# Performance work log

Hardware: AMD Instinct MI355X
Metric: run time of the kernel (lower is better)

## Reference

```python
import jax, jax.numpy as jnp
import numpy as np

N, IN, H, C, E = 20000, 256, 256, 16, 640000

def sage_conv(x, edge_index, W_l, b_l, W_r):
    # PyG SAGEConv (aggr='mean', root_weight=True):
    # out = lin_l(mean_{j in N(i)} x_j) + lin_r(x_i)
    src, dst = edge_index[0], edge_index[1]
    n = x.shape[0]
    msgs = x[src]                                            # [E, d] irregular gather
    agg = jax.ops.segment_sum(msgs, dst, num_segments=n)     # [N, d]
    deg = jax.ops.segment_sum(jnp.ones((msgs.shape[0],), x.dtype), dst, num_segments=n)
    agg = agg / jnp.maximum(deg, 1.0)[:, None]               # mean aggregation
    return agg @ W_l + b_l + x @ W_r


def setup_inputs() -> dict:
    key = jax.random.key(0)
    ks = jax.random.split(key, 10)
    s = lambda k, fi, fo: jax.random.normal(k, (fi, fo), jnp.float32) / np.sqrt(fi)
    return {
        "x": jax.random.normal(ks[0], (N, IN), jnp.float32),
        "edge_index": jax.random.randint(ks[1], (2, E), 0, N, jnp.int64),
        "W1l": s(ks[2], IN, H), "b1": jnp.zeros((H,), jnp.float32), "W1r": s(ks[3], IN, H),
        "W2l": s(ks[4], H, H),  "b2": jnp.zeros((H,), jnp.float32), "W2r": s(ks[5], H, H),
        "Wc": s(ks[6], H, C),   "bc": jnp.zeros((C,), jnp.float32),
    }


def reference(x, edge_index, W1l, b1, W1r, W2l, b2, W2r, Wc, bc):
    h = sage_conv(x, edge_index, W1l, b1, W1r)
    h = jax.nn.relu(h)                    # dropout is identity in eval mode
    z = sage_conv(h, edge_index, W2l, b2, W2r)
    return z @ Wc + bc                    # classifier logits [N, C]
```

## Files before the change

### kernel.cpp

```cpp
#include <hip/hip_runtime.h>
#include <hip/hip_bf16.h>


#define FEAT 256
#define NCLS 16
#define ZPAD 264
#define NSH  8
#define SCAP 64
#define SLOTS (NSH * SCAP)
#define CAPTOT 128

typedef __bf16 bf16x8 __attribute__((ext_vector_type(8)));
typedef __bf16 bf16x4 __attribute__((ext_vector_type(4)));
typedef float  f32x4  __attribute__((ext_vector_type(4)));
typedef float  f32x2  __attribute__((ext_vector_type(2)));
typedef unsigned int uint4v __attribute__((ext_vector_type(4)));

#define ACC8(S, U) do {                                                   \
    _Pragma("unroll")                                                     \
    for (int w_ = 0; w_ < 4; ++w_) {                                      \
        f32x2 lo_ = __builtin_amdgcn_cvt_pk_f32_fp8(U[w_], false);        \
        f32x2 hi_ = __builtin_amdgcn_cvt_pk_f32_fp8(U[w_], true);         \
        S[w_][0] += lo_[0]; S[w_][1] += lo_[1];                           \
        S[w_][2] += hi_[0]; S[w_][3] += hi_[1];                           \
    } } while (0)

__device__ __forceinline__ void load_entries(
    const int* __restrict__ cnt, const unsigned short* __restrict__ bucket,
    int node, int lane, int& e0, int& e1, int& deg, float& inv)
{
    int4 ca = *(const int4*)(cnt + node * NSH);
    int4 cb = *(const int4*)(cnt + node * NSH + 4);
    int cs[NSH] = {ca.x, ca.y, ca.z, ca.w, cb.x, cb.y, cb.z, cb.w};
    int ctrue = 0, d = 0;
    #pragma unroll
    for (int s = 0; s < NSH; ++s) {
        ctrue += cs[s];
        cs[s] = cs[s] < SCAP ? cs[s] : SCAP;
        d += cs[s];
    }
    deg = d < CAPTOT ? d : CAPTOT;
    inv = ctrue > 0 ? 1.0f / (float)ctrue : 0.0f;
    const unsigned short* lst = bucket + (size_t)node * SLOTS;

    auto get = [&](int i) -> int {
        int s = 0, loc = i;
        #pragma unroll
        for (int t = 0; t < NSH - 1; ++t) {
            if (s == t && loc >= cs[t]) { loc -= cs[t]; s = t + 1; }
        }
        return lst[s * SCAP + loc];
    };
    e0 = (lane < deg)      ? get(lane)      : 0;
    e1 = (lane + 64 < deg) ? get(lane + 64) : 0;
}


__global__ void combo_kernel(const float* __restrict__ x,
                             const float* __restrict__ W1l, const float* __restrict__ W1r,
                             const float* __restrict__ W2l, const float* __restrict__ W2r,
                             const float* __restrict__ Wc, const float* __restrict__ b2,
                             const float* __restrict__ bc,
                             const int* __restrict__ src, const int* __restrict__ dst,
                             __bf16* __restrict__ xb, unsigned char* __restrict__ x8,
                             __bf16* __restrict__ W1lT, __bf16* __restrict__ W1rT,
                             __bf16* __restrict__ WaT, __bf16* __restrict__ WbT,
                             float* __restrict__ bc2,
                             int* __restrict__ cnt, unsigned short* __restrict__ bucket,
                             int n4, int E, int nb_cvt) {
    int t = threadIdx.x;
    int bx = blockIdx.x;
    if (bx < nb_cvt) {
        int i = bx * 256 + t;
        if (i < n4) {
            f32x4 v = ((const f32x4*)x)[i];
            bf16x4 o;
            #pragma unroll
            for (int j = 0; j < 4; ++j) o[j] = (__bf16)v[j];
            ((bf16x4*)xb)[i] = o;
            int pk = 0;
            pk = __builtin_amdgcn_cvt_pk_fp8_f32(v[0], v[1], pk, false);
            pk = __builtin_amdgcn_cvt_pk_fp8_f32(v[2], v[3], pk, true);
            ((int*)x8)[i] = pk;
        }
    } else if (bx < nb_cvt + 512) {
        int b = bx - nb_cvt;
        int w = b >> 8, nn = b & 255;
        const float* W = w ? W1r : W1l;
        __bf16* WT = w ? W1rT : W1lT;
        WT[nn * FEAT + t] = (__bf16)W[t * FEAT + nn];
    } else if (bx < nb_cvt + 512 + 32) {
        int b = bx - nb_cvt - 512;
        int c = b & 15;
        const float* W = (b < 16) ? W2l : W2r;
        __bf16* WT = (b < 16) ? WaT : WbT;
        float s = 0.f;
        #pragma unroll 4
        for (int m = 0; m < FEAT; ++m)
            s += W[t * FEAT + m] * Wc[m * NCLS + c];
        WT[c * FEAT + t] = (__bf16)s;
    } else if (bx == nb_cvt + 512 + 32) {
        if (t < NCLS) {
            float s = 0.f;
            for (int k = 0; k < FEAT; ++k) s += b2[k] * Wc[k * NCLS + t];
            bc2[t] = s + bc[t];
        }
    } else {
        int sh = bx & (NSH - 1);
        int idx = (bx - nb_cvt - 512 - 33) * 256 + t;
        int e2 = idx * 2;
        if (e2 < E) {
            int2 sv = *(const int2*)(src + e2);
            int2 dv = *(const int2*)(dst + e2);
            int p0 = atomicAdd(&cnt[dv.x * NSH + sh], 1);
            if (p0 < SCAP) bucket[(size_t)dv.x * SLOTS + sh * SCAP + p0] = (unsigned short)sv.x;
            if (e2 + 1 < E) {
                int p1 = atomicAdd(&cnt[dv.y * NSH + sh], 1);
                if (p1 < SCAP) bucket[(size_t)dv.y * SLOTS + sh * SCAP + p1] = (unsigned short)sv.y;
            }
        }
    }
}


__global__ __launch_bounds__(256) void agg_fp8_kernel(
    const unsigned char* __restrict__ t8, const int* __restrict__ cnt,
    const unsigned short* __restrict__ bucket, __bf16* __restrict__ out, int n)
{
    int wave = threadIdx.x >> 6;
    int node = blockIdx.x * 4 + wave;
    if (node >= n) return;
    int lane = threadIdx.x & 63;
    int quad = lane >> 4, l16 = lane & 15;

    int e0, e1, deg; float inv;
    load_entries(cnt, bucket, node, lane, e0, e1, deg, inv);

    f32x4 s0[4], s1[4];
    #pragma unroll
    for (int w = 0; w < 4; ++w) { s0[w] = (f32x4){0.f,0.f,0.f,0.f}; s1[w] = (f32x4){0.f,0.f,0.f,0.f}; }

    int nfull = deg >> 2;
    int rem   = deg & 3;
    const unsigned char* base = t8 + l16 * 16;

    int tt = 0;
    for (; tt + 3 < nfull; tt += 4) {
        int i0 = (tt + 0) * 4 + quad, i1 = (tt + 1) * 4 + quad;
        int i2 = (tt + 2) * 4 + quad, i3 = (tt + 3) * 4 + quad;
        int j0 = (i0 < 64) ? __shfl(e0, i0) : __shfl(e1, i0 - 64);
        int j1 = (i1 < 64) ? __shfl(e0, i1) : __shfl(e1, i1 - 64);
        int j2 = (i2 < 64) ? __shfl(e0, i2) : __shfl(e1, i2 - 64);
        int j3 = (i3 < 64) ? __shfl(e0, i3) : __shfl(e1, i3 - 64);
        uint4v u0 = *(const uint4v*)(base + (size_t)j0 * FEAT);
        uint4v u1 = *(const uint4v*)(base + (size_t)j1 * FEAT);
        uint4v u2 = *(const uint4v*)(base + (size_t)j2 * FEAT);
        uint4v u3 = *(const uint4v*)(base + (size_t)j3 * FEAT);
        ACC8(s0, u0); ACC8(s1, u1); ACC8(s0, u2); ACC8(s1, u3);
    }
    for (; tt < nfull; ++tt) {
        int i = tt * 4 + quad;
        int j = (i < 64) ? __shfl(e0, i) : __shfl(e1, i - 64);
        uint4v u = *(const uint4v*)(base + (size_t)j * FEAT);
        ACC8(s0, u);
    }
    if (rem) {
        int i = nfull * 4 + quad;
        int j = (i < 64) ? __shfl(e0, i) : __shfl(e1, i - 64);
        if (quad < rem) {
            uint4v u = *(const uint4v*)(base + (size_t)j * FEAT);
            ACC8(s1, u);
        }
    }

    #pragma unroll
    for (int w = 0; w < 4; ++w)
        #pragma unroll
        for (int j = 0; j < 4; ++j) {
            float v = s0[w][j] + s1[w][j];
            v += __shfl_xor(v, 16, 64);
            v += __shfl_xor(v, 32, 64);
            s0[w][j] = v;
        }

    bf16x4 o;
    #pragma unroll
    for (int j = 0; j < 4; ++j) o[j] = (__bf16)(s0[quad][j] * inv);
    *(bf16x4*)(out + (size_t)node * FEAT + l16 * 16 + quad * 4) = o;
}


__global__ __launch_bounds__(256) void gemm1_kernel(
    const __bf16* __restrict__ A1, const __bf16* __restrict__ A2,
    const __bf16* __restrict__ B1T, const __bf16* __restrict__ B2T,
    const float* __restrict__ bias,
    const __bf16* __restrict__ WaT, const __bf16* __restrict__ WbT,
    const float* __restrict__ bc2,
    __bf16* __restrict__ pb, float* __restrict__ q, int M)
{
    __shared__ __align__(16) __bf16 tile[32][ZPAD];

    int m0   = blockIdx.x * 32;
    int lane = threadIdx.x & 63;
    int wave = threadIdx.x >> 6;
    int l16  = lane & 15, quad = lane >> 4;

    f32x4 acc[2][4];
    #pragma unroll
    for (int a = 0; a < 2; ++a)
        #pragma unroll
        for (int b = 0; b < 4; ++b) acc[a][b] = (f32x4){0.f, 0.f, 0.f, 0.f};

    int arow[2];
    #pragma unroll
    for (int mt = 0; mt < 2; ++mt) {
        int r = m0 + mt * 16 + l16;
        arow[mt] = (r < M) ? r : (M - 1);
    }
    int nbase = wave * 64;

    for (int pass = 0; pass < 2; ++pass) {
        const __bf16* A  = pass ? A2 : A1;
        const __bf16* BT = pass ? B2T : B1T;
        #pragma unroll 2
        for (int kk = 0; kk < 8; ++kk) {
            int k0 = kk * 32 + quad * 8;
            bf16x8 af[2], bfm[4];
            #pragma unroll
            for (int mt = 0; mt < 2; ++mt)
                af[mt] = *(const bf16x8*)(A + (size_t)arow[mt] * FEAT + k0);
            #pragma unroll
            for (int nt = 0; nt < 4; ++nt)
                bfm[nt] = *(const bf16x8*)(BT + (size_t)(nbase + nt * 16 + l16) * FEAT + k0);
            #pragma unroll
            for (int mt = 0; mt < 2; ++mt)
                #pragma unroll
                for (int nt = 0; nt < 4; ++nt)
                    acc[mt][nt] = __builtin_amdgcn_mfma_f32_16x16x32_bf16(
                        af[mt], bfm[nt], acc[mt][nt], 0, 0, 0);
        }
    }

    #pragma unroll
    for (int nt = 0; nt < 4; ++nt) {
        int col = nbase + nt * 16 + l16;
        float bv = bias[col];
        #pragma unroll
        for (int mt = 0; mt < 2; ++mt) {
            int lr = mt * 16 + quad * 4;
            #pragma unroll
            for (int r = 0; r < 4; ++r) {
                float v = acc[mt][nt][r] + bv;
                tile[lr + r][col] = (__bf16)(v > 0.f ? v : 0.f);
            }
        }
    }
    __syncthreads();

    {
        int half = wave >> 1;
        int lr = half * 16 + l16;
        const __bf16* WT = (wave & 1) ? WbT : WaT;
        f32x4 a = {0.f, 0.f, 0.f, 0.f};
        #pragma unroll
        for (int kk = 0; kk < 8; ++kk) {
            int k0 = kk * 32 + quad * 8;
            bf16x8 av = *(const bf16x8*)(&tile[lr][k0]);
            bf16x8 bv = *(const bf16x8*)(WT + (size_t)l16 * FEAT + k0);
            a = __builtin_amdgcn_mfma_f32_16x16x32_bf16(av, bv, a, 0, 0, 0);
        }
        if (wave & 1) {
            float qv = bc2[l16];
            #pragma unroll
            for (int r = 0; r < 4; ++r) {
                int row = m0 + half * 16 + quad * 4 + r;
                if (row < M) q[(size_t)row * NCLS + l16] = a[r] + qv;
            }
        } else {
            #pragma unroll
            for (int r = 0; r < 4; ++r) {
                int row = m0 + half * 16 + quad * 4 + r;
                if (row < M) pb[(size_t)row * NCLS + l16] = (__bf16)a[r];
            }
        }
    }
}


__global__ __launch_bounds__(256) void agg_out_kernel(
    const __bf16* __restrict__ pb, const float* __restrict__ q,
    const int* __restrict__ cnt, const unsigned short* __restrict__ bucket,
    float* __restrict__ out, int n)
{
    int wave = threadIdx.x >> 6;
    int node = blockIdx.x * 4 + wave;
    if (node >= n) return;
    int lane = threadIdx.x & 63;
    int quad = lane >> 4, l16 = lane & 15;

    int e0, e1, deg; float inv;
    load_entries(cnt, bucket, node, lane, e0, e1, deg, inv);

    float s0 = 0.f, s1 = 0.f;
    int nfull = deg >> 2;
    int rem   = deg & 3;

    int tt = 0;
    for (; tt + 3 < nfull; tt += 4) {
        int i0 = (tt + 0) * 4 + quad, i1 = (tt + 1) * 4 + quad;
        int i2 = (tt + 2) * 4 + quad, i3 = (tt + 3) * 4 + quad;
        int j0 = (i0 < 64) ? __shfl(e0, i0) : __shfl(e1, i0 - 64);
        int j1 = (i1 < 64) ? __shfl(e0, i1) : __shfl(e1, i1 - 64);
        int j2 = (i2 < 64) ? __shfl(e0, i2) : __shfl(e1, i2 - 64);
        int j3 = (i3 < 64) ? __shfl(e0, i3) : __shfl(e1, i3 - 64);
        float v0 = (float)pb[(size_t)j0 * NCLS + l16];
        float v1 = (float)pb[(size_t)j1 * NCLS + l16];
        float v2 = (float)pb[(size_t)j2 * NCLS + l16];
        float v3 = (float)pb[(size_t)j3 * NCLS + l16];
        s0 += v0 + v1;
        s1 += v2 + v3;
    }
    for (; tt < nfull; ++tt) {
        int i = tt * 4 + quad;
        int j = (i < 64) ? __shfl(e0, i) : __shfl(e1, i - 64);
        s0 += (float)pb[(size_t)j * NCLS + l16];
    }
    if (rem) {
        int i = nfull * 4 + quad;
        int j = (i < 64) ? __shfl(e0, i) : __shfl(e1, i - 64);
        if (quad < rem) s1 += (float)pb[(size_t)j * NCLS + l16];
    }

    float v = s0 + s1;
    v += __shfl_xor(v, 16, 64);
    v += __shfl_xor(v, 32, 64);

    if (quad == 0) {
        out[(size_t)node * NCLS + l16] = v * inv + q[(size_t)node * NCLS + l16];
    }
}


extern "C" void kernel_launch(void* const* d_in, const int* in_sizes, int n_in,
                              void* d_out, int out_size, void* d_ws, size_t ws_size,
                              hipStream_t stream) {
    const float* x   = (const float*)d_in[0];
    const int*   ei  = (const int*)d_in[1];
    const float* W1l = (const float*)d_in[2];
    const float* b1  = (const float*)d_in[3];
    const float* W1r = (const float*)d_in[4];
    const float* W2l = (const float*)d_in[5];
    const float* b2  = (const float*)d_in[6];
    const float* W2r = (const float*)d_in[7];
    const float* Wc  = (const float*)d_in[8];
    const float* bc  = (const float*)d_in[9];
    float* out = (float*)d_out;

    const int n = in_sizes[0] / FEAT;
    const int E = in_sizes[1] / 2;
    const int* srcp = ei;
    const int* dstp = ei + E;

    char* p = (char*)d_ws;
    auto alloc = [&](size_t bytes) { char* r = p; p += (bytes + 511) & ~511ull; return r; };
    int* cnt       = (int*)alloc((size_t)n * NSH * 4);
    unsigned short* bucket = (unsigned short*)alloc((size_t)n * SLOTS * 2);
    __bf16* W1lT   = (__bf16*)alloc((size_t)FEAT * FEAT * 2);
    __bf16* W1rT   = (__bf16*)alloc((size_t)FEAT * FEAT * 2);
    __bf16* WaT    = (__bf16*)alloc((size_t)NCLS * FEAT * 2);
    __bf16* WbT    = (__bf16*)alloc((size_t)NCLS * FEAT * 2);
    float*  bc2    = (float*)alloc((size_t)NCLS * 4);
    __bf16* xb     = (__bf16*)alloc((size_t)n * FEAT * 2);
    unsigned char* x8 = (unsigned char*)alloc((size_t)n * FEAT);
    __bf16* aggb   = (__bf16*)alloc((size_t)n * FEAT * 2);
    __bf16* pb     = (__bf16*)alloc((size_t)n * NCLS * 2);
    float*  qb     = (float*)alloc((size_t)n * NCLS * 4);

    int n4 = n * FEAT / 4;
    int nb_cvt  = (n4 + 255) / 256;
    int nb_edge = (E + 511) / 512;

    hipMemsetAsync(cnt, 0, (size_t)n * NSH * 4, stream);

    combo_kernel<<<nb_cvt + 512 + 32 + 1 + nb_edge, 256, 0, stream>>>(
        x, W1l, W1r, W2l, W2r, Wc, b2, bc, srcp, dstp,
        xb, x8, W1lT, W1rT, WaT, WbT, bc2, cnt, bucket, n4, E, nb_cvt);

    agg_fp8_kernel<<<(n + 3) / 4, 256, 0, stream>>>(x8, cnt, bucket, aggb, n);
    gemm1_kernel<<<(n + 31) / 32, 256, 0, stream>>>(aggb, xb, W1lT, W1rT, b1,
                                                    WaT, WbT, bc2, pb, qb, n);

    agg_out_kernel<<<(n + 3) / 4, 256, 0, stream>>>(pb, qb, cnt, bucket, out, n);
}
```

Baseline: 195.7 us.

## Fuse first-layer FP8 neighbor aggregation into GEMM kernel via shared-memory tile

Merges the aggregation kernel into the first GEMM kernel. Each block first aggregates its 32 nodes' neighbor features (8 per wave) into a shared-memory bf16 tile, then runs the lin_l MFMA pass from LDS and the lin_r pass from global memory. This drops the bf16 aggregate buffer write/read round trip and one kernel launch. In exchange, parallelism for the latency-bound gather drops: the grid has 8x fewer blocks and each wave handles 8 nodes serially, which may hurt latency hiding.

Result: slower. 221.2 us (+13.0%).

```diff
diff --git a/kernel.cpp b/kernel.cpp
--- a/kernel.cpp
+++ b/kernel.cpp
@@ -123,75 +123,10 @@
 }
 
 
-__global__ __launch_bounds__(256) void agg_fp8_kernel(
+__global__ __launch_bounds__(256) void agg_gemm_kernel(
     const unsigned char* __restrict__ t8, const int* __restrict__ cnt,
-    const unsigned short* __restrict__ bucket, __bf16* __restrict__ out, int n)
-{
-    int wave = threadIdx.x >> 6;
-    int node = blockIdx.x * 4 + wave;
-    if (node >= n) return;
-    int lane = threadIdx.x & 63;
-    int quad = lane >> 4, l16 = lane & 15;
-
-    int e0, e1, deg; float inv;
-    load_entries(cnt, bucket, node, lane, e0, e1, deg, inv);
-
-    f32x4 s0[4], s1[4];
-    #pragma unroll
-    for (int w = 0; w < 4; ++w) { s0[w] = (f32x4){0.f,0.f,0.f,0.f}; s1[w] = (f32x4){0.f,0.f,0.f,0.f}; }
-
-    int nfull = deg >> 2;
-    int rem   = deg & 3;
-    const unsigned char* base = t8 + l16 * 16;
-
-    int tt = 0;
-    for (; tt + 3 < nfull; tt += 4) {
-        int i0 = (tt + 0) * 4 + quad, i1 = (tt + 1) * 4 + quad;
-        int i2 = (tt + 2) * 4 + quad, i3 = (tt + 3) * 4 + quad;
-        int j0 = (i0 < 64) ? __shfl(e0, i0) : __shfl(e1, i0 - 64);
-        int j1 = (i1 < 64) ? __shfl(e0, i1) : __shfl(e1, i1 - 64);
-        int j2 = (i2 < 64) ? __shfl(e0, i2) : __shfl(e1, i2 - 64);
-        int j3 = (i3 < 64) ? __shfl(e0, i3) : __shfl(e1, i3 - 64);
-        uint4v u0 = *(const uint4v*)(base + (size_t)j0 * FEAT);
-        uint4v u1 = *(const uint4v*)(base + (size_t)j1 * FEAT);
-        uint4v u2 = *(const uint4v*)(base + (size_t)j2 * FEAT);
-        uint4v u3 = *(const uint4v*)(base + (size_t)j3 * FEAT);
-        ACC8(s0, u0); ACC8(s1, u1); ACC8(s0, u2); ACC8(s1, u3);
-    }
-    for (; tt < nfull; ++tt) {
-        int i = tt * 4 + quad;
-        int j = (i < 64) ? __shfl(e0, i) : __shfl(e1, i - 64);
-        uint4v u = *(const uint4v*)(base + (size_t)j * FEAT);
-        ACC8(s0, u);
-    }
-    if (rem) {
-        int i = nfull * 4 + quad;
-        int j = (i < 64) ? __shfl(e0, i) : __shfl(e1, i - 64);
-        if (quad < rem) {
-            uint4v u = *(const uint4v*)(base + (size_t)j * FEAT);
-            ACC8(s1, u);
-        }
-    }
-
-    #pragma unroll
-    for (int w = 0; w < 4; ++w)
-        #pragma unroll
-        for (int j = 0; j < 4; ++j) {
-            float v = s0[w][j] + s1[w][j];
-            v += __shfl_xor(v, 16, 64);
-            v += __shfl_xor(v, 32, 64);
-            s0[w][j] = v;
-        }
-
-    bf16x4 o;
-    #pragma unroll
-    for (int j = 0; j < 4; ++j) o[j] = (__bf16)(s0[quad][j] * inv);
-    *(bf16x4*)(out + (size_t)node * FEAT + l16 * 16 + quad * 4) = o;
-}
-
-
-__global__ __launch_bounds__(256) void gemm1_kernel(
-    const __bf16* __restrict__ A1, const __bf16* __restrict__ A2,
+    const unsigned short* __restrict__ bucket,
+    const __bf16* __restrict__ A2,
     const __bf16* __restrict__ B1T, const __bf16* __restrict__ B2T,
     const float* __restrict__ bias,
     const __bf16* __restrict__ WaT, const __bf16* __restrict__ WbT,
@@ -205,6 +140,72 @@
     int wave = threadIdx.x >> 6;
     int l16  = lane & 15, quad = lane >> 4;
 
+    #pragma unroll 1
+    for (int nd = 0; nd < 8; ++nd) {
+        int row  = wave * 8 + nd;
+        int node = m0 + row;
+        if (node < M) {
+            int e0, e1, deg; float inv;
+            load_entries(cnt, bucket, node, lane, e0, e1, deg, inv);
+
+            f32x4 s0[4], s1[4];
+            #pragma unroll
+            for (int w = 0; w < 4; ++w) { s0[w] = (f32x4){0.f,0.f,0.f,0.f}; s1[w] = (f32x4){0.f,0.f,0.f,0.f}; }
+
+            int nfull = deg >> 2;
+            int rem   = deg & 3;
+            const unsigned char* base = t8 + l16 * 16;
+
+            int tt = 0;
+            for (; tt + 3 < nfull; tt += 4) {
+                int i0 = (tt + 0) * 4 + quad, i1 = (tt + 1) * 4 + quad;
+                int i2 = (tt + 2) * 4 + quad, i3 = (tt + 3) * 4 + quad;
+                int j0 = (i0 < 64) ? __shfl(e0, i0) : __shfl(e1, i0 - 64);
+                int j1 = (i1 < 64) ? __shfl(e0, i1) : __shfl(e1, i1 - 64);
+                int j2 = (i2 < 64) ? __shfl(e0, i2) : __shfl(e1, i2 - 64);
+                int j3 = (i3 < 64) ? __shfl(e0, i3) : __shfl(e1, i3 - 64);
+                uint4v u0 = *(const uint4v*)(base + (size_t)j0 * FEAT);
+                uint4v u1 = *(const uint4v*)(base + (size_t)j1 * FEAT);
+                uint4v u2 = *(const uint4v*)(base + (size_t)j2 * FEAT);
+                uint4v u3 = *(const uint4v*)(base + (size_t)j3 * FEAT);
+                ACC8(s0, u0); ACC8(s1, u1); ACC8(s0, u2); ACC8(s1, u3);
+            }
+            for (; tt < nfull; ++tt) {
+                int i = tt * 4 + quad;
+                int j = (i < 64) ? __shfl(e0, i) : __shfl(e1, i - 64);
+                uint4v u = *(const uint4v*)(base + (size_t)j * FEAT);
+                ACC8(s0, u);
+            }
+            if (rem) {
+                int i = nfull * 4 + quad;
+                int j = (i < 64) ? __shfl(e0, i) : __shfl(e1, i - 64);
+                if (quad < rem) {
+                    uint4v u = *(const uint4v*)(base + (size_t)j * FEAT);
+                    ACC8(s1, u);
+                }
+            }
+
+            #pragma unroll
+            for (int w = 0; w < 4; ++w)
+                #pragma unroll
+                for (int j = 0; j < 4; ++j) {
+                    float v = s0[w][j] + s1[w][j];
+                    v += __shfl_xor(v, 16, 64);
+                    v += __shfl_xor(v, 32, 64);
+                    s0[w][j] = v;
+                }
+
+            bf16x4 o;
+            #pragma unroll
+            for (int j = 0; j < 4; ++j) o[j] = (__bf16)(s0[quad][j] * inv);
+            *(bf16x4*)(&tile[row][l16 * 16 + quad * 4]) = o;
+        } else {
+            bf16x4 z = (bf16x4){(__bf16)0.f, (__bf16)0.f, (__bf16)0.f, (__bf16)0.f};
+            *(bf16x4*)(&tile[row][l16 * 16 + quad * 4]) = z;
+        }
+    }
+    __syncthreads();
+
     f32x4 acc[2][4];
     #pragma unroll
     for (int a = 0; a < 2; ++a)
@@ -219,26 +220,41 @@
     }
     int nbase = wave * 64;
 
-    for (int pass = 0; pass < 2; ++pass) {
-        const __bf16* A  = pass ? A2 : A1;
-        const __bf16* BT = pass ? B2T : B1T;
-        #pragma unroll 2
-        for (int kk = 0; kk < 8; ++kk) {
-            int k0 = kk * 32 + quad * 8;
-            bf16x8 af[2], bfm[4];
-            #pragma unroll
-            for (int mt = 0; mt < 2; ++mt)
-                af[mt] = *(const bf16x8*)(A + (size_t)arow[mt] * FEAT + k0);
+    #pragma unroll 2
+    for (int kk = 0; kk < 8; ++kk) {
+        int k0 = kk * 32 + quad * 8;
+        bf16x8 af[2], bfm[4];
+        #pragma unroll
+        for (int mt = 0; mt < 2; ++mt)
+            af[mt] = *(const bf16x8*)(&tile[mt * 16 + l16][k0]);
+        #pragma unroll
+        for (int nt = 0; nt < 4; ++nt)
+            bfm[nt] = *(const bf16x8*)(B1T + (size_t)(nbase + nt * 16 + l16) * FEAT + k0);
+        #pragma unroll
+        for (int mt = 0; mt < 2; ++mt)
             #pragma unroll
             for (int nt = 0; nt < 4; ++nt)
-                bfm[nt] = *(const bf16x8*)(BT + (size_t)(nbase + nt * 16 + l16) * FEAT + k0);
-            #pragma unroll
-            for (int mt = 0; mt < 2; ++mt)
-                #pragma unroll
-                for (int nt = 0; nt < 4; ++nt)
-                    acc[mt][nt] = __builtin_amdgcn_mfma_f32_16x16x32_bf16(
-                        af[mt], bfm[nt], acc[mt][nt], 0, 0, 0);
-        }
+                acc[mt][nt] = __builtin_amdgcn_mfma_f32_16x16x32_bf16(
+                    af[mt], bfm[nt], acc[mt][nt], 0, 0, 0);
+    }
+    __syncthreads();
+
+    #pragma unroll 2
+    for (int kk = 0; kk < 8; ++kk) {
+        int k0 = kk * 32 + quad * 8;
+        bf16x8 af[2], bfm[4];
+        #pragma unroll
+        for (int mt = 0; mt < 2; ++mt)
+            af[mt] = *(const bf16x8*)(A2 + (size_t)arow[mt] * FEAT + k0);
+        #pragma unroll
+        for (int nt = 0; nt < 4; ++nt)
+            bfm[nt] = *(const bf16x8*)(B2T + (size_t)(nbase + nt * 16 + l16) * FEAT + k0);
+        #pragma unroll
+        for (int mt = 0; mt < 2; ++mt)
+            #pragma unroll
+            for (int nt = 0; nt < 4; ++nt)
+                acc[mt][nt] = __builtin_amdgcn_mfma_f32_16x16x32_bf16(
+                    af[mt], bfm[nt], acc[mt][nt], 0, 0, 0);
     }
 
     #pragma unroll
@@ -372,7 +388,6 @@
     float*  bc2    = (float*)alloc((size_t)NCLS * 4);
     __bf16* xb     = (__bf16*)alloc((size_t)n * FEAT * 2);
     unsigned char* x8 = (unsigned char*)alloc((size_t)n * FEAT);
-    __bf16* aggb   = (__bf16*)alloc((size_t)n * FEAT * 2);
     __bf16* pb     = (__bf16*)alloc((size_t)n * NCLS * 2);
     float*  qb     = (float*)alloc((size_t)n * NCLS * 4);
 
@@ -386,9 +401,8 @@
         x, W1l, W1r, W2l, W2r, Wc, b2, bc, srcp, dstp,
         xb, x8, W1lT, W1rT, WaT, WbT, bc2, cnt, bucket, n4, E, nb_cvt);
 
-    agg_fp8_kernel<<<(n + 3) / 4, 256, 0, stream>>>(x8, cnt, bucket, aggb, n);
-    gemm1_kernel<<<(n + 31) / 32, 256, 0, stream>>>(aggb, xb, W1lT, W1rT, b1,
-                                                    WaT, WbT, bc2, pb, qb, n);
+    agg_gemm_kernel<<<(n + 31) / 32, 256, 0, stream>>>(
+        x8, cnt, bucket, xb, W1lT, W1rT, b1, WaT, WbT, bc2, pb, qb, n);
 
     agg_out_kernel<<<(n + 3) / 4, 256, 0, stream>>>(pb, qb, cnt, bucket, out, n);
 }
```

## Fuse all stages into one cooperative persistent kernel with grid syncs

Applied to the files above, without the earlier changes.

Replaces the memset and four separate kernel launches with a single cooperative persistent kernel. Inside it, grid-stride loops run each stage and grid.sync() separates them. The aim is to remove launch and inter-kernel gap overhead. The old multi-kernel path stays as a fallback if the cooperative launch fails. It also skips the second bucket lookup when degree is at most 64. The trade-off is a fixed grid size capped at 2048 blocks, grid-wide barrier cost, and possibly lower occupancy, since the fused kernel carries the GEMM's shared tile and register pressure into every stage.

Result: slower. 480.5 us (+145.6%).

```diff
diff --git a/kernel.cpp b/kernel.cpp
--- a/kernel.cpp
+++ b/kernel.cpp
@@ -1,5 +1,8 @@
 #include <hip/hip_runtime.h>
 #include <hip/hip_bf16.h>
+#include <hip/hip_cooperative_groups.h>
+
+namespace cg = cooperative_groups;
 
 
 #define FEAT 256
@@ -51,25 +54,28 @@
         }
         return lst[s * SCAP + loc];
     };
-    e0 = (lane < deg)      ? get(lane)      : 0;
-    e1 = (lane + 64 < deg) ? get(lane + 64) : 0;
-}
-
-
-__global__ void combo_kernel(const float* __restrict__ x,
-                             const float* __restrict__ W1l, const float* __restrict__ W1r,
-                             const float* __restrict__ W2l, const float* __restrict__ W2r,
-                             const float* __restrict__ Wc, const float* __restrict__ b2,
-                             const float* __restrict__ bc,
-                             const int* __restrict__ src, const int* __restrict__ dst,
-                             __bf16* __restrict__ xb, unsigned char* __restrict__ x8,
-                             __bf16* __restrict__ W1lT, __bf16* __restrict__ W1rT,
-                             __bf16* __restrict__ WaT, __bf16* __restrict__ WbT,
-                             float* __restrict__ bc2,
-                             int* __restrict__ cnt, unsigned short* __restrict__ bucket,
-                             int n4, int E, int nb_cvt) {
-    int t = threadIdx.x;
-    int bx = blockIdx.x;
+    e0 = (lane < deg) ? get(lane) : 0;
+    e1 = 0;
+    if (deg > 64)
+        e1 = (lane + 64 < deg) ? get(lane + 64) : 0;
+}
+
+
+__device__ __forceinline__ void combo_body(
+    int bx, int t,
+    const float* __restrict__ x,
+    const float* __restrict__ W1l, const float* __restrict__ W1r,
+    const float* __restrict__ W2l, const float* __restrict__ W2r,
+    const float* __restrict__ Wc, const float* __restrict__ b2,
+    const float* __restrict__ bc,
+    const int* __restrict__ src, const int* __restrict__ dst,
+    __bf16* __restrict__ xb, unsigned char* __restrict__ x8,
+    __bf16* __restrict__ W1lT, __bf16* __restrict__ W1rT,
+    __bf16* __restrict__ WaT, __bf16* __restrict__ WbT,
+    float* __restrict__ bc2,
+    int* __restrict__ cnt, unsigned short* __restrict__ bucket,
+    int n4, int E, int nb_cvt)
+{
     if (bx < nb_cvt) {
         int i = bx * 256 + t;
         if (i < n4) {
@@ -122,17 +128,13 @@
     }
 }
 
-
-__global__ __launch_bounds__(256) void agg_fp8_kernel(
+__device__ __forceinline__ void agg1_body(
+    int node, int t,
     const unsigned char* __restrict__ t8, const int* __restrict__ cnt,
-    const unsigned short* __restrict__ bucket, __bf16* __restrict__ out, int n)
-{
-    int wave = threadIdx.x >> 6;
-    int node = blockIdx.x * 4 + wave;
-    if (node >= n) return;
-    int lane = threadIdx.x & 63;
+    const unsigned short* __restrict__ bucket, __bf16* __restrict__ aggb)
+{
+    int lane = t & 63;
     int quad = lane >> 4, l16 = lane & 15;
-
     int e0, e1, deg; float inv;
     load_entries(cnt, bucket, node, lane, e0, e1, deg, inv);
 
@@ -186,11 +188,11 @@
     bf16x4 o;
     #pragma unroll
     for (int j = 0; j < 4; ++j) o[j] = (__bf16)(s0[quad][j] * inv);
-    *(bf16x4*)(out + (size_t)node * FEAT + l16 * 16 + quad * 4) = o;
-}
-
-
-__global__ __launch_bounds__(256) void gemm1_kernel(
+    *(bf16x4*)(aggb + (size_t)node * FEAT + l16 * 16 + quad * 4) = o;
+}
+
+__device__ __forceinline__ void gemm_body(
+    int m0, int t, __bf16 (*tile)[ZPAD],
     const __bf16* __restrict__ A1, const __bf16* __restrict__ A2,
     const __bf16* __restrict__ B1T, const __bf16* __restrict__ B2T,
     const float* __restrict__ bias,
@@ -198,11 +200,8 @@
     const float* __restrict__ bc2,
     __bf16* __restrict__ pb, float* __restrict__ q, int M)
 {
-    __shared__ __align__(16) __bf16 tile[32][ZPAD];
-
-    int m0   = blockIdx.x * 32;
-    int lane = threadIdx.x & 63;
-    int wave = threadIdx.x >> 6;
+    int lane = t & 63;
+    int wave = t >> 6;
     int l16  = lane & 15, quad = lane >> 4;
 
     f32x4 acc[2][4];
@@ -284,20 +283,17 @@
             }
         }
     }
-}
-
-
-__global__ __launch_bounds__(256) void agg_out_kernel(
+    __syncthreads();
+}
+
+__device__ __forceinline__ void aggout_body(
+    int node, int t,
     const __bf16* __restrict__ pb, const float* __restrict__ q,
     const int* __restrict__ cnt, const unsigned short* __restrict__ bucket,
-    float* __restrict__ out, int n)
-{
-    int wave = threadIdx.x >> 6;
-    int node = blockIdx.x * 4 + wave;
-    if (node >= n) return;
-    int lane = threadIdx.x & 63;
+    float* __restrict__ out)
+{
+    int lane = t & 63;
     int quad = lane >> 4, l16 = lane & 15;
-
     int e0, e1, deg; float inv;
     load_entries(cnt, bucket, node, lane, e0, e1, deg, inv);
 
@@ -341,6 +337,92 @@
 }
 
 
+__global__ __launch_bounds__(256, 4) void mega_kernel(
+    const float* x, const float* W1l, const float* W1r,
+    const float* W2l, const float* W2r, const float* Wc,
+    const float* b1, const float* b2, const float* bc,
+    const int* src, const int* dst,
+    __bf16* xb, unsigned char* x8,
+    __bf16* W1lT, __bf16* W1rT, __bf16* WaT, __bf16* WbT, float* bc2,
+    int* cnt, unsigned short* bucket,
+    __bf16* aggb, __bf16* pb, float* qb, float* out,
+    int n, int E)
+{
+    cg::grid_group grid = cg::this_grid();
+    __shared__ __align__(16) __bf16 tile[32][ZPAD];
+
+    int t    = threadIdx.x;
+    int bid  = blockIdx.x;
+    int nblk = gridDim.x;
+    int wave = t >> 6;
+
+    int n4      = n * (FEAT / 4);
+    int nb_cvt  = (n4 + 255) >> 8;
+    int nb_edge = (E + 511) >> 9;
+    int nvb     = nb_cvt + 512 + 32 + 1 + nb_edge;
+
+    for (int i = bid * 256 + t; i < n * NSH; i += nblk * 256) cnt[i] = 0;
+    grid.sync();
+
+    for (int bx = bid; bx < nvb; bx += nblk)
+        combo_body(bx, t, x, W1l, W1r, W2l, W2r, Wc, b2, bc, src, dst,
+                   xb, x8, W1lT, W1rT, WaT, WbT, bc2, cnt, bucket, n4, E, nb_cvt);
+    grid.sync();
+
+    for (int node = bid * 4 + wave; node < n; node += nblk * 4)
+        agg1_body(node, t, x8, cnt, bucket, aggb);
+    grid.sync();
+
+    int ntile = (n + 31) >> 5;
+    for (int mt0 = bid; mt0 < ntile; mt0 += nblk)
+        gemm_body(mt0 * 32, t, tile, aggb, xb, W1lT, W1rT, b1,
+                  WaT, WbT, bc2, pb, qb, n);
+    grid.sync();
+
+    for (int node = bid * 4 + wave; node < n; node += nblk * 4)
+        aggout_body(node, t, pb, qb, cnt, bucket, out);
+}
+
+
+__global__ void combo_kernel(const float* x, const float* W1l, const float* W1r,
+                             const float* W2l, const float* W2r, const float* Wc,
+                             const float* b2, const float* bc,
+                             const int* src, const int* dst,
+                             __bf16* xb, unsigned char* x8,
+                             __bf16* W1lT, __bf16* W1rT,
+                             __bf16* WaT, __bf16* WbT, float* bc2,
+                             int* cnt, unsigned short* bucket,
+                             int n4, int E, int nb_cvt) {
+    combo_body(blockIdx.x, threadIdx.x, x, W1l, W1r, W2l, W2r, Wc, b2, bc,
+               src, dst, xb, x8, W1lT, W1rT, WaT, WbT, bc2, cnt, bucket,
+               n4, E, nb_cvt);
+}
+
+__global__ __launch_bounds__(256) void agg_fp8_kernel(
+    const unsigned char* t8, const int* cnt, const unsigned short* bucket,
+    __bf16* aggb, int n) {
+    int node = blockIdx.x * 4 + (threadIdx.x >> 6);
+    if (node < n) agg1_body(node, threadIdx.x, t8, cnt, bucket, aggb);
+}
+
+__global__ __launch_bounds__(256) void gemm1_kernel(
+    const __bf16* A1, const __bf16* A2,
+    const __bf16* B1T, const __bf16* B2T, const float* bias,
+    const __bf16* WaT, const __bf16* WbT, const float* bc2,
+    __bf16* pb, float* q, int M) {
+    __shared__ __align__(16) __bf16 tile[32][ZPAD];
+    gemm_body(blockIdx.x * 32, threadIdx.x, tile, A1, A2, B1T, B2T, bias,
+              WaT, WbT, bc2, pb, q, M);
+}
+
+__global__ __launch_bounds__(256) void agg_out_kernel(
+    const __bf16* pb, const float* q, const int* cnt,
+    const unsigned short* bucket, float* out, int n) {
+    int node = blockIdx.x * 4 + (threadIdx.x >> 6);
+    if (node < n) aggout_body(node, threadIdx.x, pb, q, cnt, bucket, out);
+}
+
+
 extern "C" void kernel_launch(void* const* d_in, const int* in_sizes, int n_in,
                               void* d_out, int out_size, void* d_ws, size_t ws_size,
                               hipStream_t stream) {
@@ -356,8 +438,8 @@
     const float* bc  = (const float*)d_in[9];
     float* out = (float*)d_out;
 
-    const int n = in_sizes[0] / FEAT;
-    const int E = in_sizes[1] / 2;
+    int n = in_sizes[0] / FEAT;
+    int E = in_sizes[1] / 2;
     const int* srcp = ei;
     const int* dstp = ei + E;
 
@@ -380,15 +462,36 @@
     int nb_cvt  = (n4 + 255) / 256;
     int nb_edge = (E + 511) / 512;
 
-    hipMemsetAsync(cnt, 0, (size_t)n * NSH * 4, stream);
-
-    combo_kernel<<<nb_cvt + 512 + 32 + 1 + nb_edge, 256, 0, stream>>>(
-        x, W1l, W1r, W2l, W2r, Wc, b2, bc, srcp, dstp,
-        xb, x8, W1lT, W1rT, WaT, WbT, bc2, cnt, bucket, n4, E, nb_cvt);
-
-    agg_fp8_kernel<<<(n + 3) / 4, 256, 0, stream>>>(x8, cnt, bucket, aggb, n);
-    gemm1_kernel<<<(n + 31) / 32, 256, 0, stream>>>(aggb, xb, W1lT, W1rT, b1,
-                                                    WaT, WbT, bc2, pb, qb, n);
-
-    agg_out_kernel<<<(n + 3) / 4, 256, 0, stream>>>(pb, qb, cnt, bucket, out, n);
-}
+    static int coopGrid = 0;
+    if (coopGrid == 0) {
+        int nb = 0;
+        if (hipOccupancyMaxActiveBlocksPerMultiprocessor(&nb, mega_kernel, 256, 0)
+                != hipSuccess || nb < 1)
+            nb = 4;
+        long g = (long)nb * 256;
+        if (g > 2048) g = 2048;
+        coopGrid = (int)(g & ~7L);
+        if (coopGrid < 8) coopGrid = 8;
+    }
+
+    void* args[] = {
+        (void*)&x, (void*)&W1l, (void*)&W1r, (void*)&W2l, (void*)&W2r, (void*)&Wc,
+        (void*)&b1, (void*)&b2, (void*)&bc, (void*)&srcp, (void*)&dstp,
+        (void*)&xb, (void*)&x8, (void*)&W1lT, (void*)&W1rT, (void*)&WaT, (void*)&WbT,
+        (void*)&bc2, (void*)&cnt, (void*)&bucket, (void*)&aggb, (void*)&pb,
+        (void*)&qb, (void*)&out, (void*)&n, (void*)&E };
+
+    hipError_t err = hipLaunchCooperativeKernel(
+        mega_kernel, dim3(coopGrid), dim3(256), args, 0, stream);
+
+    if (err != hipSuccess) {
+        hipMemsetAsync(cnt, 0, (size_t)n * NSH * 4, stream);
+        combo_kernel<<<nb_cvt + 512 + 32 + 1 + nb_edge, 256, 0, stream>>>(
+            x, W1l, W1r, W2l, W2r, Wc, b2, bc, srcp, dstp,
+            xb, x8, W1lT, W1rT, WaT, WbT, bc2, cnt, bucket, n4, E, nb_cvt);
+        agg_fp8_kernel<<<(n + 3) / 4, 256, 0, stream>>>(x8, cnt, bucket, aggb, n);
+        gemm1_kernel<<<(n + 31) / 32, 256, 0, stream>>>(aggb, xb, W1lT, W1rT, b1,
+                                                        WaT, WbT, bc2, pb, qb, n);
+        agg_out_kernel<<<(n + 3) / 4, 256, 0, stream>>>(pb, qb, cnt, bucket, out, n);
+    }
+}
```
